# Kernel optimization log

Hardware: AMD Instinct MI355X
Metric: run time of the kernel (lower is better)

## Reference

```python
import jax, jax.numpy as jnp
import numpy as np

V = 1024      # token vocab
C = 8         # n_codebooks
T = 256       # seg_len
BP = 4        # block_pairs (n_latent_blocks)
K = 512       # latent_vocab_size (codebook entries)
E = 128       # emb_dim
D = 128       # latent_dim / d_model
BETA = 0.05
NB = 6 * BP   # decoder sequence length = 24
NH = 4
HD = D // NH
FF = 512
R = 8
IN_FLAT = NB * D
OUT = T * C * V
B = 32


def setup_inputs() -> dict:
    key = jax.random.key(0)
    ks = jax.random.split(key, 20)
    n = lambda i, shape, s=0.02: jax.random.normal(ks[i], shape, jnp.float32) * s
    return {
        "tokens_prev": jax.random.randint(ks[0], (B, T, C), 0, V, jnp.int32),
        "tokens_curr": jax.random.randint(ks[1], (B, T, C), 0, V, jnp.int32),
        "tokens_next": jax.random.randint(ks[2], (B, T, C), 0, V, jnp.int32),
        "emb": n(3, (V, E)),
        "conv1_w": n(4, (4 * D, E * C, 3)),
        "conv1_b": jnp.zeros((4 * D,), jnp.float32),
        "conv2_w": n(5, (2 * D, 4 * D, 1)),
        "conv2_b": jnp.zeros((2 * D,), jnp.float32),
        "cb_instru": jax.random.uniform(ks[6], (K, D), jnp.float32, -1.0 / K, 1.0 / K),
        "cb_vocal": jax.random.uniform(ks[7], (K, D), jnp.float32, -1.0 / K, 1.0 / K),
        "pos": n(8, (1, NB, D), 1.0),
        "attn_in_w": n(9, (3 * D, D)),
        "attn_in_b": jnp.zeros((3 * D,), jnp.float32),
        "attn_out_w": n(10, (D, D)),
        "attn_out_b": jnp.zeros((D,), jnp.float32),
        "ln1_g": jnp.ones((D,), jnp.float32),
        "ln1_b": jnp.zeros((D,), jnp.float32),
        "lin1_w": n(11, (FF, D)),
        "lin1_b": jnp.zeros((FF,), jnp.float32),
        "lin2_w": n(12, (D, FF)),
        "lin2_b": jnp.zeros((D,), jnp.float32),
        "ln2_g": jnp.ones((D,), jnp.float32),
        "ln2_b": jnp.zeros((D,), jnp.float32),
        "lora_a": n(13, (R, IN_FLAT), 0.01),
        "lora_b": n(14, (OUT, R), 0.01),
    }


def _conv1d(x, w, b, pad):
    # x: (B, Cin, L), w: (Cout, Cin, Kw)
    y = jax.lax.conv_general_dilated(x, w, window_strides=(1,), padding=[(pad, pad)],
                                     dimension_numbers=("NCH", "OIH", "NCH"))
    return y + b[None, :, None]


def _encode(tokens, emb, w1, b1, w2, b2):
    Bb, Tt, Cc = tokens.shape
    x = emb[tokens].reshape(Bb, Tt, -1).transpose(0, 2, 1)       # (B, C*E, T)
    x = jax.nn.relu(_conv1d(x, w1, b1, 1))                        # (B, 4D, T)
    x = jax.nn.relu(_conv1d(x, w2, b2, 0))                        # (B, 2D, T)
    # AdaptiveAvgPool1d(BP) with T % BP == 0 -> mean over contiguous chunks
    x = x.reshape(Bb, 2 * D, BP, Tt // BP).mean(-1).transpose(0, 2, 1)  # (B, BP, 2D)
    return x[..., :D], x[..., D:]


def _vq(z, codebook):
    # z: (B, N, D); eval-mode VQ (no EMA update)
    Bb, N, Dd = z.shape
    flat = z.reshape(-1, Dd)
    dist = (jnp.sum(flat * flat, axis=1, keepdims=True)
            - 2.0 * flat @ codebook.T
            + jnp.sum(codebook * codebook, axis=1))
    codes = jnp.argmin(dist, axis=1)
    z_q = codebook[codes].reshape(Bb, N, Dd)
    commit = jnp.mean((z - jax.lax.stop_gradient(z_q)) ** 2)
    loss = BETA * commit
    z_q_st = z + jax.lax.stop_gradient(z_q - z)
    return z_q_st, codes.reshape(Bb, N), loss


def _layer_norm(x, g, b):
    mu = x.mean(-1, keepdims=True)
    var = ((x - mu) ** 2).mean(-1, keepdims=True)
    return (x - mu) * jax.lax.rsqrt(var + 1e-5) * g + b


def _tf_layer(x, in_w, in_b, out_w, out_b, g1, b1, w1, bb1, w2, bb2, g2, b2):
    # Post-norm TransformerEncoderLayer (relu, eval/no-dropout). x: (B, S, D)
    Bb, S, Dd = x.shape
    qkv = x @ in_w.T + in_b
    q, k, v = jnp.split(qkv, 3, axis=-1)
    q = q.reshape(Bb, S, NH, HD).transpose(0, 2, 1, 3)
    k = k.reshape(Bb, S, NH, HD).transpose(0, 2, 1, 3)
    v = v.reshape(Bb, S, NH, HD).transpose(0, 2, 1, 3)
    attn = jax.nn.softmax(jnp.einsum("bhsd,bhtd->bhst", q, k) / np.sqrt(HD), axis=-1)
    o = jnp.einsum("bhst,bhtd->bhsd", attn, v).transpose(0, 2, 1, 3).reshape(Bb, S, Dd)
    x = _layer_norm(x + o @ out_w.T + out_b, g1, b1)
    ff = jax.nn.relu(x @ w1.T + bb1) @ w2.T + bb2
    return _layer_norm(x + ff, g2, b2)


def reference(tokens_prev, tokens_curr, tokens_next, emb, conv1_w, conv1_b,
              conv2_w, conv2_b, cb_instru, cb_vocal, pos, attn_in_w, attn_in_b,
              attn_out_w, attn_out_b, ln1_g, ln1_b, lin1_w, lin1_b, lin2_w,
              lin2_b, ln2_g, ln2_b, lora_a, lora_b):
    p_i, p_v = _encode(tokens_prev, emb, conv1_w, conv1_b, conv2_w, conv2_b)
    c_i, c_v = _encode(tokens_curr, emb, conv1_w, conv1_b, conv2_w, conv2_b)
    n_i, n_v = _encode(tokens_next, emb, conv1_w, conv1_b, conv2_w, conv2_b)
    p_i_q, _, l1 = _vq(p_i, cb_instru)
    c_i_q, _, l2 = _vq(c_i, cb_instru)
    n_i_q, _, l3 = _vq(n_i, cb_instru)
    p_v_q, _, l4 = _vq(p_v, cb_vocal)
    c_v_q, _, l5 = _vq(c_v, cb_vocal)
    n_v_q, _, l6 = _vq(n_v, cb_vocal)
    vq_loss = l1 + l2 + l3 + l4 + l5 + l6
    z = jnp.concatenate([p_i_q, p_v_q, c_i_q, c_v_q, n_i_q, n_v_q], axis=1)  # (B, 24, D)
    z = z + pos[:, :z.shape[1], :]
    z = _tf_layer(z, attn_in_w, attn_in_b, attn_out_w, attn_out_b,
                  ln1_g, ln1_b, lin1_w, lin1_b, lin2_w, lin2_b, ln2_g, ln2_b)
    Bb = z.shape[0]
    flat = z.reshape(Bb, -1)
    logits = (flat @ lora_a.T) @ lora_b.T          # (B, T*C*V)
    logits = logits.reshape(Bb, T, C, V)
    logp = jax.nn.log_softmax(logits, axis=-1)
    nll = -jnp.take_along_axis(logp, tokens_curr[..., None].astype(jnp.int32), axis=-1)
    recon_loss = nll.mean()
    total_loss = recon_loss + vq_loss
    return total_loss
```

## Files before the change

### kernel.cpp

```cpp
#include <hip/hip_runtime.h>
#include <hip/hip_bf16.h>
#include <cstdint>
#include <cstddef>

typedef __attribute__((ext_vector_type(8))) short short8;
typedef __attribute__((ext_vector_type(4))) float floatx4;


__device__ __forceinline__ ushort f2bf(float f) {
    union { float f; unsigned int u; } x; x.f = f;
    unsigned int r = (x.u + 0x7fffu + ((x.u >> 16) & 1u)) >> 16;
    return (ushort)r;
}
__device__ __forceinline__ float bf2f(ushort u) {
    union { unsigned int u; float f; } x; x.u = ((unsigned int)u) << 16;
    return x.f;
}

__global__ __launch_bounds__(256) void prep_all(
    const float* __restrict__ emb, const float* __restrict__ w1,
    const float* __restrict__ w2, const float* __restrict__ cbi,
    const float* __restrict__ cbv, const float* __restrict__ aiw,
    const float* __restrict__ aow, const float* __restrict__ l1w,
    const float* __restrict__ l2w,
    ushort* __restrict__ ebf, ushort* __restrict__ w1bf, ushort* __restrict__ w2bf,
    float* __restrict__ cbiT, float* __restrict__ cbvT,
    ushort* __restrict__ aiwbf, ushort* __restrict__ aowbf,
    ushort* __restrict__ l1wbf, ushort* __restrict__ l2wbf,
    float* __restrict__ accum)
{
    int idx = blockIdx.x * 256 + threadIdx.x;
    if (idx < 4) accum[idx] = 0.f;
    if (idx < 131072) {
        ebf[idx] = f2bf(emb[idx]);
    } else if (idx < 262144) {
        int j = idx - 131072; w2bf[j] = f2bf(w2[j]);
    } else if (idx < 327680) {
        int j = idx - 262144; cbiT[(j & 127) * 512 + (j >> 7)] = cbi[j];
    } else if (idx < 393216) {
        int j = idx - 327680; cbvT[(j & 127) * 512 + (j >> 7)] = cbv[j];
    } else if (idx < 442368) {
        int j = idx - 393216; aiwbf[j] = f2bf(aiw[j]);
    } else if (idx < 475136) {
        int j = idx - 442368; aowbf[j] = f2bf(aow[j]);
    } else if (idx < 540672) {
        int j = idx - 475136; l1wbf[j] = f2bf(l1w[j]);
    } else if (idx < 606208) {
        int j = idx - 540672; l2wbf[j] = f2bf(l2w[j]);
    } else if (idx < 2179072) {
        int j = idx - 606208;
        int e  = j & 127;
        int co = (j >> 7) & 511;
        int cc = (j >> 16) & 7;
        int kw = j >> 19;
        w1bf[j] = f2bf(w1[(co * 1024 + cc * 128 + e) * 3 + kw]);
    }
}

__global__ __launch_bounds__(512, 4) void conv1_mfma(
    const int* __restrict__ tp, const int* __restrict__ tcu, const int* __restrict__ tn,
    const ushort* __restrict__ ebf, const ushort* __restrict__ w1bf,
    const float* __restrict__ b1, ushort* __restrict__ y1)
{
    constexpr int LDA = 136;
    __shared__ ushort As[130 * LDA];
    __shared__ ushort Bs[128 * LDA];
    __shared__ int tokL[130 * 8];
    const int tid = threadIdx.x;
    const int bx = blockIdx.x;
    const int nb = bx & 3, mb = bx >> 2;
    const int set = mb >> 6, rem = mb & 63, bb = rem >> 1, t0 = (rem & 1) << 7;
    const int n0 = nb << 7;
    const int* tok = (set == 0) ? tp : ((set == 1) ? tcu : tn);

    for (int idx = tid; idx < 1040; idx += 512) {
        const int row = idx >> 3, cc = idx & 7;
        const int gt = t0 + row - 1;
        tokL[idx] = (gt >= 0 && gt < 256) ? tok[bb * 2048 + gt * 8 + cc] : -1;
    }

    const int w = tid >> 6, lane = tid & 63;
    const int wm = w & 1, wn = w >> 1;
    const int rA = lane & 15, q4 = lane >> 4;
    const int ch = tid & 15, rowst = tid >> 4;

    floatx4 acc[4][2];
    for (int mi = 0; mi < 4; ++mi)
        for (int ni = 0; ni < 2; ++ni)
            acc[mi][ni] = (floatx4)(0.0f);

    __syncthreads();

    for (int cc = 0; cc < 8; ++cc) {
        for (int p = 0; p < 5; ++p) {
            const int row = p * 32 + rowst;
            if (row < 130) {
                const int tk = tokL[row * 8 + cc];
                uint4 val = make_uint4(0u, 0u, 0u, 0u);
                if (tk >= 0) val = *(const uint4*)(ebf + tk * 128 + ch * 8);
                *(uint4*)(As + row * LDA + ch * 8) = val;
            }
        }
        for (int kw = 0; kw < 3; ++kw) {
            const ushort* wsrc = w1bf + ((size_t)((kw * 8 + cc) * 512 + n0)) * 128;
            for (int p = 0; p < 4; ++p) {
                const int row = p * 32 + rowst;
                *(uint4*)(Bs + row * LDA + ch * 8) = *(const uint4*)(wsrc + row * 128 + ch * 8);
            }
            __syncthreads();
            for (int ks = 0; ks < 4; ++ks) {
                const int k0 = ks * 32 + q4 * 8;
                short8 a[4], bfr[2];
                for (int mi = 0; mi < 4; ++mi)
                    a[mi] = *(const short8*)(As + (wm * 64 + mi * 16 + rA + kw) * LDA + k0);
                for (int ni = 0; ni < 2; ++ni)
                    bfr[ni] = *(const short8*)(Bs + (wn * 32 + ni * 16 + rA) * LDA + k0);
                for (int mi = 0; mi < 4; ++mi)
                    for (int ni = 0; ni < 2; ++ni)
                        acc[mi][ni] = __builtin_amdgcn_mfma_f32_16x16x32_bf16(
                            a[mi], bfr[ni], acc[mi][ni], 0, 0, 0);
            }
            __syncthreads();
        }
    }
    for (int ni = 0; ni < 2; ++ni) {
        const int co = n0 + wn * 32 + ni * 16 + rA;
        const float bias = b1[co];
        for (int mi = 0; mi < 4; ++mi) {
            for (int r = 0; r < 4; ++r) {
                const int t = t0 + wm * 64 + mi * 16 + q4 * 4 + r;
                float v = acc[mi][ni][r] + bias;
                v = v > 0.f ? v : 0.f;
                y1[((size_t)(set * 32 + bb) * 256 + t) * 512 + co] = f2bf(v);
            }
        }
    }
}

__global__ __launch_bounds__(512, 4) void conv2_mfma(
    const ushort* __restrict__ y1, const ushort* __restrict__ w2bf,
    const float* __restrict__ b2, float* __restrict__ y2)
{
    constexpr int LDA = 136;
    __shared__ ushort As[128 * LDA];
    __shared__ ushort Bs[128 * LDA];
    __shared__ float pool[256];
    const int tid = threadIdx.x;
    const int bx = blockIdx.x;
    const int nb = bx & 1, mb = bx >> 1;
    const int set = mb >> 6, rem = mb & 63, bb = rem >> 1, t0 = (rem & 1) << 7;
    const int n0 = nb << 7;
    const int w = tid >> 6, lane = tid & 63;
    const int wm = w & 1, wn = w >> 1;
    const int rA = lane & 15, q4 = lane >> 4;
    const int ch = tid & 15, rowst = tid >> 4;

    floatx4 acc[4][2];
    for (int mi = 0; mi < 4; ++mi)
        for (int ni = 0; ni < 2; ++ni)
            acc[mi][ni] = (floatx4)(0.0f);

    const size_t arowbase = ((size_t)(set * 32 + bb) * 256 + t0) * 512;
    for (int kc = 0; kc < 4; ++kc) {
        for (int p = 0; p < 4; ++p) {
            const int row = p * 32 + rowst;
            *(uint4*)(As + row * LDA + ch * 8) =
                *(const uint4*)(y1 + arowbase + (size_t)row * 512 + kc * 128 + ch * 8);
            *(uint4*)(Bs + row * LDA + ch * 8) =
                *(const uint4*)(w2bf + (size_t)(n0 + row) * 512 + kc * 128 + ch * 8);
        }
        __syncthreads();
        for (int ks = 0; ks < 4; ++ks) {
            const int k0 = ks * 32 + q4 * 8;
            short8 a[4], bfr[2];
            for (int mi = 0; mi < 4; ++mi)
                a[mi] = *(const short8*)(As + (wm * 64 + mi * 16 + rA) * LDA + k0);
            for (int ni = 0; ni < 2; ++ni)
                bfr[ni] = *(const short8*)(Bs + (wn * 32 + ni * 16 + rA) * LDA + k0);
            for (int mi = 0; mi < 4; ++mi)
                for (int ni = 0; ni < 2; ++ni)
                    acc[mi][ni] = __builtin_amdgcn_mfma_f32_16x16x32_bf16(
                        a[mi], bfr[ni], acc[mi][ni], 0, 0, 0);
        }
        __syncthreads();
    }
    for (int ni = 0; ni < 2; ++ni) {
        const int col = wn * 32 + ni * 16 + rA;
        const float bias = b2[n0 + col];
        float s = 0.f;
        for (int mi = 0; mi < 4; ++mi)
            for (int r = 0; r < 4; ++r) {
                float v = acc[mi][ni][r] + bias;
                s += v > 0.f ? v : 0.f;
            }
        s += __shfl_xor(s, 16);
        s += __shfl_xor(s, 32);
        if (q4 == 0) pool[wm * 128 + col] = s;
    }
    __syncthreads();
    if (tid < 256) {
        const int wrow = tid >> 7, col = tid & 127;
        const int p = (t0 >> 6) + wrow;
        y2[((size_t)(set * 32 + bb) * 4 + p) * 256 + n0 + col] = pool[tid] * (1.f / 64.f);
    }
}

__global__ __launch_bounds__(256) void vq_kernel(
    const float* __restrict__ y2, const float* __restrict__ cbiT, const float* __restrict__ cbvT,
    const float* __restrict__ cbi, const float* __restrict__ cbv,
    const float* __restrict__ pos, float* __restrict__ ztr, float* __restrict__ accum)
{
    const int q = blockIdx.x;
    const int tid = threadIdx.x;
    const int set = q >> 7, bb = (q >> 2) & 31, p = q & 3;
    __shared__ float zloc[256];
    __shared__ float bestv[4];
    __shared__ int   besti[4];
    __shared__ int   code_sh[2];
    __shared__ float wsum2[4];
    zloc[tid] = y2[(size_t)q * 256 + tid];
    __syncthreads();
    const int w = tid >> 6, lane = tid & 63;
    const int half = w >> 1, sub = w & 1;
    const float4* cbT4 = (const float4*)(half ? cbvT : cbiT);
    const float* zh = zloc + half * 128;
    const int k4 = sub * 64 + lane;
    float a0 = 0.f, a1 = 0.f, a2 = 0.f, a3 = 0.f;
    for (int d = 0; d < 128; ++d) {
        float4 v = cbT4[d * 128 + k4];
        const float z = zh[d];
        float d0 = z - v.x, d1 = z - v.y, d2 = z - v.z, d3 = z - v.w;
        a0 += d0 * d0; a1 += d1 * d1; a2 += d2 * d2; a3 += d3 * d3;
    }
    float best = a0; int bidx = k4 * 4;
    if (a1 < best) { best = a1; bidx = k4 * 4 + 1; }
    if (a2 < best) { best = a2; bidx = k4 * 4 + 2; }
    if (a3 < best) { best = a3; bidx = k4 * 4 + 3; }
    for (int off = 32; off > 0; off >>= 1) {
        float ov = __shfl_xor(best, off);
        int   oi = __shfl_xor(bidx, off);
        if (ov < best || (ov == best && oi < bidx)) { best = ov; bidx = oi; }
    }
    if (lane == 0) { bestv[w] = best; besti[w] = bidx; }
    __syncthreads();
    if (tid < 2) {
        float v0 = bestv[tid * 2], v1 = bestv[tid * 2 + 1];
        int   i0 = besti[tid * 2], i1 = besti[tid * 2 + 1];
        code_sh[tid] = (v1 < v0 || (v1 == v0 && i1 < i0)) ? i1 : i0;
    }
    __syncthreads();
    const int hh = tid >> 7, d = tid & 127;
    const int code = code_sh[hh];
    const float* cb = hh ? cbv : cbi;
    const float zq = cb[code * 128 + d];
    const float diff = zloc[hh * 128 + d] - zq;
    float sq = diff * diff;
    for (int off = 32; off > 0; off >>= 1) sq += __shfl_xor(sq, off);
    if (lane == 0) wsum2[w] = sq;
    const int s = (set * 2 + hh) * 4 + p;
    ztr[((size_t)bb * 24 + s) * 128 + d] = zq + pos[s * 128 + d];
    __syncthreads();
    if (tid == 0) atomicAdd(&accum[0], wsum2[0] + wsum2[1] + wsum2[2] + wsum2[3]);
}

__global__ __launch_bounds__(256) void tail_kernel(
    const float* __restrict__ ztr,
    const ushort* __restrict__ aiwbf, const float* __restrict__ aib,
    const ushort* __restrict__ aowbf, const float* __restrict__ aob,
    const float* __restrict__ g1, const float* __restrict__ be1,
    const ushort* __restrict__ l1wbf, const float* __restrict__ l1b,
    const ushort* __restrict__ l2wbf, const float* __restrict__ l2b,
    const float* __restrict__ g2, const float* __restrict__ be2,
    const float* __restrict__ lora_a, float* __restrict__ hbuf)
{
    __shared__ __align__(16) char LDSC[162304];
    float*  Xf  = (float*)LDSC;
    ushort* Abf = (ushort*)(LDSC + 12288);
    char*   S   = LDSC + 20992;
    ushort* Wq  = (ushort*)S;
    float*  QKV = (float*)(S + 104448);
    float*  Ssc = (float*)S;
    ushort* Wo  = (ushort*)S;
    ushort* W1  = (ushort*)S;
    ushort* Hbf = (ushort*)S;
    ushort* Wh  = (ushort*)(S + 34304);
    float*  ps  = (float*)(S + 104448);
    float*  pq  = (float*)(S + 104960);
    float*  muv = (float*)(S + 105472);
    float*  inv = (float*)(S + 105600);

    const int b = blockIdx.x;
    const int tid = threadIdx.x;
    const int w = tid >> 6, lane = tid & 63;
    const int rA = lane & 15, q4 = lane >> 4;

    for (int i = tid; i < 544; i += 256) ((uint4*)Abf)[i] = make_uint4(0u, 0u, 0u, 0u);
    __syncthreads();
    for (int i = tid; i < 3072; i += 256) {
        float v = ztr[(size_t)b * 3072 + i];
        Xf[i] = v;
        Abf[(i >> 7) * 136 + (i & 127)] = f2bf(v);
    }
    for (int i = tid; i < 6144; i += 256) {
        const int row = i >> 4, ch = i & 15;
        *(uint4*)(Wq + row * 136 + ch * 8) = *(const uint4*)(aiwbf + row * 128 + ch * 8);
    }
    __syncthreads();

    {
        floatx4 acc[2][6];
        for (int mi = 0; mi < 2; ++mi) for (int ni = 0; ni < 6; ++ni) acc[mi][ni] = (floatx4)(0.f);
        for (int ks = 0; ks < 4; ++ks) {
            const int k0 = ks * 32 + q4 * 8;
            short8 a[2];
            for (int mi = 0; mi < 2; ++mi)
                a[mi] = *(const short8*)(Abf + (mi * 16 + rA) * 136 + k0);
            for (int ni = 0; ni < 6; ++ni) {
                short8 bfr = *(const short8*)(Wq + ((w * 6 + ni) * 16 + rA) * 136 + k0);
                for (int mi = 0; mi < 2; ++mi)
                    acc[mi][ni] = __builtin_amdgcn_mfma_f32_16x16x32_bf16(a[mi], bfr, acc[mi][ni], 0, 0, 0);
            }
        }
        for (int ni = 0; ni < 6; ++ni) {
            const int col = (w * 6 + ni) * 16 + rA;
            const float bs = aib[col];
            for (int mi = 0; mi < 2; ++mi)
                for (int r = 0; r < 4; ++r) {
                    const int row = mi * 16 + q4 * 4 + r;
                    if (row < 24) QKV[row * 384 + col] = acc[mi][ni][r] + bs;
                }
        }
    }
    __syncthreads();

    {
        const int h = w;
        for (int l = 0; l < 9; ++l) {
            const int e = l * 64 + lane;
            const int i = e / 24, j = e - i * 24;
            float s = 0.f;
            for (int d = 0; d < 32; ++d)
                s += QKV[i * 384 + h * 32 + d] * QKV[j * 384 + 128 + h * 32 + d];
            Ssc[w * 576 + i * 24 + j] = s * 0.17677669529663687f;
        }
        __syncthreads();
        if (lane < 24) {
            float* row = Ssc + w * 576 + lane * 24;
            float m = row[0];
            for (int j = 1; j < 24; ++j) m = row[j] > m ? row[j] : m;
            float ssum = 0.f;
            for (int j = 0; j < 24; ++j) { float e = __expf(row[j] - m); row[j] = e; ssum += e; }
            float iv = 1.f / ssum;
            for (int j = 0; j < 24; ++j) row[j] *= iv;
        }
        __syncthreads();
        for (int l = 0; l < 12; ++l) {
            const int idx = l * 64 + lane;
            const int s = idx >> 5, d = idx & 31;
            float a = 0.f;
            for (int j = 0; j < 24; ++j)
                a += Ssc[w * 576 + s * 24 + j] * QKV[j * 384 + 256 + h * 32 + d];
            Abf[s * 136 + h * 32 + d] = f2bf(a);
        }
    }
    __syncthreads();

    for (int i = tid; i < 2048; i += 256) {
        const int row = i >> 4, ch = i & 15;
        *(uint4*)(Wo + row * 136 + ch * 8) = *(const uint4*)(aowbf + row * 128 + ch * 8);
    }
    __syncthreads();
    {
        floatx4 acc[2][2];
        for (int mi = 0; mi < 2; ++mi) for (int ni = 0; ni < 2; ++ni) acc[mi][ni] = (floatx4)(0.f);
        for (int ks = 0; ks < 4; ++ks) {
            const int k0 = ks * 32 + q4 * 8;
            short8 a[2];
            for (int mi = 0; mi < 2; ++mi)
                a[mi] = *(const short8*)(Abf + (mi * 16 + rA) * 136 + k0);
            for (int ni = 0; ni < 2; ++ni) {
                short8 bfr = *(const short8*)(Wo + ((w * 2 + ni) * 16 + rA) * 136 + k0);
                for (int mi = 0; mi < 2; ++mi)
                    acc[mi][ni] = __builtin_amdgcn_mfma_f32_16x16x32_bf16(a[mi], bfr, acc[mi][ni], 0, 0, 0);
            }
        }
        for (int ni = 0; ni < 2; ++ni) {
            const int col = (w * 2 + ni) * 16 + rA;
            const float bs = aob[col];
            for (int mi = 0; mi < 2; ++mi)
                for (int r = 0; r < 4; ++r) {
                    const int row = mi * 16 + q4 * 4 + r;
                    acc[mi][ni][r] += bs + (row < 24 ? Xf[row * 128 + col] : 0.f);
                }
        }
        for (int mi = 0; mi < 2; ++mi)
            for (int r = 0; r < 4; ++r) {
                float s  = acc[mi][0][r] + acc[mi][1][r];
                float sq = acc[mi][0][r] * acc[mi][0][r] + acc[mi][1][r] * acc[mi][1][r];
                for (int off = 1; off < 16; off <<= 1) { s += __shfl_xor(s, off); sq += __shfl_xor(sq, off); }
                if (rA == 0) { const int rl = mi * 16 + q4 * 4 + r; ps[rl * 4 + w] = s; pq[rl * 4 + w] = sq; }
            }
        __syncthreads();
        if (tid < 32) {
            float s  = ps[tid * 4] + ps[tid * 4 + 1] + ps[tid * 4 + 2] + ps[tid * 4 + 3];
            float sq = pq[tid * 4] + pq[tid * 4 + 1] + pq[tid * 4 + 2] + pq[tid * 4 + 3];
            float mu = s * (1.f / 128.f);
            float var = sq * (1.f / 128.f) - mu * mu;
            muv[tid] = mu; inv[tid] = rsqrtf(var + 1e-5f);
        }
        __syncthreads();
        for (int ni = 0; ni < 2; ++ni) {
            const int col = (w * 2 + ni) * 16 + rA;
            const float gg = g1[col], bb2 = be1[col];
            for (int mi = 0; mi < 2; ++mi)
                for (int r = 0; r < 4; ++r) {
                    const int rl = mi * 16 + q4 * 4 + r;
                    if (rl < 24) {
                        float v = (acc[mi][ni][r] - muv[rl]) * inv[rl] * gg + bb2;
                        Xf[rl * 128 + col] = v;
                        Abf[rl * 136 + col] = f2bf(v);
                    }
                }
        }
    }
    __syncthreads();

    for (int i = tid; i < 8192; i += 256) {
        const int row = i >> 4, ch = i & 15;
        *(uint4*)(W1 + row * 136 + ch * 8) = *(const uint4*)(l1wbf + row * 128 + ch * 8);
    }
    __syncthreads();
    {
        floatx4 acc[2][8];
        for (int mi = 0; mi < 2; ++mi) for (int ni = 0; ni < 8; ++ni) acc[mi][ni] = (floatx4)(0.f);
        for (int ks = 0; ks < 4; ++ks) {
            const int k0 = ks * 32 + q4 * 8;
            short8 a[2];
            for (int mi = 0; mi < 2; ++mi)
                a[mi] = *(const short8*)(Abf + (mi * 16 + rA) * 136 + k0);
            for (int ni = 0; ni < 8; ++ni) {
                short8 bfr = *(const short8*)(W1 + ((w * 8 + ni) * 16 + rA) * 136 + k0);
                for (int mi = 0; mi < 2; ++mi)
                    acc[mi][ni] = __builtin_amdgcn_mfma_f32_16x16x32_bf16(a[mi], bfr, acc[mi][ni], 0, 0, 0);
            }
        }
        __syncthreads();
        for (int i = tid; i < 536; i += 256) ((uint4*)(Hbf + 24 * 536))[i] = make_uint4(0u, 0u, 0u, 0u);
        for (int ni = 0; ni < 8; ++ni) {
            const int col = (w * 8 + ni) * 16 + rA;
            const float bs = l1b[col];
            for (int mi = 0; mi < 2; ++mi)
                for (int r = 0; r < 4; ++r) {
                    const int row = mi * 16 + q4 * 4 + r;
                    if (row < 24) {
                        float v = acc[mi][ni][r] + bs;
                        Hbf[row * 536 + col] = f2bf(v > 0.f ? v : 0.f);
                    }
                }
        }
    }
    __syncthreads();

    {
        floatx4 acc[2][2];
        for (int mi = 0; mi < 2; ++mi) for (int ni = 0; ni < 2; ++ni) acc[mi][ni] = (floatx4)(0.f);
        for (int kh = 0; kh < 2; ++kh) {
            for (int i = tid; i < 4096; i += 256) {
                const int row = i >> 5, ch = i & 31;
                *(uint4*)(Wh + row * 264 + ch * 8) =
                    *(const uint4*)(l2wbf + row * 512 + kh * 256 + ch * 8);
            }
            __syncthreads();
            for (int ks = 0; ks < 8; ++ks) {
                const int k0 = ks * 32 + q4 * 8;
                short8 a[2];
                for (int mi = 0; mi < 2; ++mi)
                    a[mi] = *(const short8*)(Hbf + (mi * 16 + rA) * 536 + kh * 256 + k0);
                for (int ni = 0; ni < 2; ++ni) {
                    short8 bfr = *(const short8*)(Wh + ((w * 2 + ni) * 16 + rA) * 264 + k0);
                    for (int mi = 0; mi < 2; ++mi)
                        acc[mi][ni] = __builtin_amdgcn_mfma_f32_16x16x32_bf16(a[mi], bfr, acc[mi][ni], 0, 0, 0);
                }
            }
            __syncthreads();
        }
        for (int ni = 0; ni < 2; ++ni) {
            const int col = (w * 2 + ni) * 16 + rA;
            const float bs = l2b[col];
            for (int mi = 0; mi < 2; ++mi)
                for (int r = 0; r < 4; ++r) {
                    const int row = mi * 16 + q4 * 4 + r;
                    acc[mi][ni][r] += bs + (row < 24 ? Xf[row * 128 + col] : 0.f);
                }
        }
        for (int mi = 0; mi < 2; ++mi)
            for (int r = 0; r < 4; ++r) {
                float s  = acc[mi][0][r] + acc[mi][1][r];
                float sq = acc[mi][0][r] * acc[mi][0][r] + acc[mi][1][r] * acc[mi][1][r];
                for (int off = 1; off < 16; off <<= 1) { s += __shfl_xor(s, off); sq += __shfl_xor(sq, off); }
                if (rA == 0) { const int rl = mi * 16 + q4 * 4 + r; ps[rl * 4 + w] = s; pq[rl * 4 + w] = sq; }
            }
        __syncthreads();
        if (tid < 32) {
            float s  = ps[tid * 4] + ps[tid * 4 + 1] + ps[tid * 4 + 2] + ps[tid * 4 + 3];
            float sq = pq[tid * 4] + pq[tid * 4 + 1] + pq[tid * 4 + 2] + pq[tid * 4 + 3];
            float mu = s * (1.f / 128.f);
            float var = sq * (1.f / 128.f) - mu * mu;
            muv[tid] = mu; inv[tid] = rsqrtf(var + 1e-5f);
        }
        __syncthreads();
        for (int ni = 0; ni < 2; ++ni) {
            const int col = (w * 2 + ni) * 16 + rA;
            const float gg = g2[col], bb2 = be2[col];
            for (int mi = 0; mi < 2; ++mi)
                for (int r = 0; r < 4; ++r) {
                    const int rl = mi * 16 + q4 * 4 + r;
                    if (rl < 24)
                        Xf[rl * 128 + col] = (acc[mi][ni][r] - muv[rl]) * inv[rl] * gg + bb2;
                }
        }
    }
    __syncthreads();

    for (int rr = 0; rr < 2; ++rr) {
        const int r = w + rr * 4;
        float a = 0.f;
        for (int i = lane; i < 3072; i += 64)
            a += lora_a[(size_t)r * 3072 + i] * Xf[i];
        for (int off = 32; off > 0; off >>= 1) a += __shfl_xor(a, off);
        if (lane == 0) hbuf[b * 8 + r] = a;
    }
}

__global__ __launch_bounds__(256) void logits_kernel(
    const float* __restrict__ hbuf, const float* __restrict__ lora_b,
    const int* __restrict__ tokc, float* __restrict__ accum, float* __restrict__ out)
{
    const int tid = threadIdx.x;
    const int tcb = blockIdx.x;
    __shared__ float hl[256];
    __shared__ float wsum[4];
    __shared__ float ltok;
    hl[tid] = hbuf[tid];
    float wr[4][8];
    for (int i = 0; i < 4; ++i) {
        const float4* pw = (const float4*)(lora_b + ((size_t)tcb * 1024 + tid + 256 * i) * 8);
        float4 x = pw[0], y = pw[1];
        wr[i][0] = x.x; wr[i][1] = x.y; wr[i][2] = x.z; wr[i][3] = x.w;
        wr[i][4] = y.x; wr[i][5] = y.y; wr[i][6] = y.z; wr[i][7] = y.w;
    }
    __syncthreads();
    float nll = 0.f;
    for (int bb = 0; bb < 32; ++bb) {
        const int tv = tokc[bb * 2048 + tcb];
        const float* h = hl + bb * 8;
        float h0 = h[0], h1 = h[1], h2 = h[2], h3 = h[3];
        float h4 = h[4], h5 = h[5], h6 = h[6], h7 = h[7];
        float sl = 0.f;
        for (int i = 0; i < 4; ++i) {
            float lg = h0 * wr[i][0] + h1 * wr[i][1] + h2 * wr[i][2] + h3 * wr[i][3]
                     + h4 * wr[i][4] + h5 * wr[i][5] + h6 * wr[i][6] + h7 * wr[i][7];
            sl += __expf(lg);
            if (tid + 256 * i == tv) ltok = lg;
        }
        for (int off = 32; off > 0; off >>= 1) sl += __shfl_xor(sl, off);
        if ((tid & 63) == 0) wsum[tid >> 6] = sl;
        __syncthreads();
        if (tid == 0) nll += logf(wsum[0] + wsum[1] + wsum[2] + wsum[3]) - ltok;
        __syncthreads();
    }
    if (tid == 0) {
        atomicAdd(&accum[1], nll);
        __threadfence();
        unsigned int prev = atomicAdd((unsigned int*)(accum + 2), 1u);
        if (prev == 2047u) {
            float vq  = atomicAdd(&accum[0], 0.f);
            float rec = atomicAdd(&accum[1], 0.f);
            out[0] = rec * (1.f / 65536.f) + 0.05f * vq * (1.f / 16384.f);
        }
    }
}

extern "C" void kernel_launch(void* const* d_in, const int* in_sizes, int n_in,
                              void* d_out, int out_size, void* d_ws, size_t ws_size,
                              hipStream_t stream) {
    const int*   tp   = (const int*)d_in[0];
    const int*   tcu  = (const int*)d_in[1];
    const int*   tn   = (const int*)d_in[2];
    const float* emb  = (const float*)d_in[3];
    const float* w1   = (const float*)d_in[4];
    const float* b1   = (const float*)d_in[5];
    const float* w2   = (const float*)d_in[6];
    const float* b2   = (const float*)d_in[7];
    const float* cbi  = (const float*)d_in[8];
    const float* cbv  = (const float*)d_in[9];
    const float* pos  = (const float*)d_in[10];
    const float* aiw  = (const float*)d_in[11];
    const float* aib  = (const float*)d_in[12];
    const float* aow  = (const float*)d_in[13];
    const float* aob  = (const float*)d_in[14];
    const float* g1   = (const float*)d_in[15];
    const float* be1  = (const float*)d_in[16];
    const float* l1w  = (const float*)d_in[17];
    const float* l1b  = (const float*)d_in[18];
    const float* l2w  = (const float*)d_in[19];
    const float* l2b  = (const float*)d_in[20];
    const float* g2   = (const float*)d_in[21];
    const float* be2  = (const float*)d_in[22];
    const float* lra  = (const float*)d_in[23];
    const float* lrb  = (const float*)d_in[24];

    char* wsb = (char*)d_ws;
    ushort* ebf  = (ushort*)(wsb + 0);
    ushort* w1bf = (ushort*)(wsb + 262144);
    ushort* w2bf = (ushort*)(wsb + 3407872);
    float*  cbiT = (float*)(wsb + 3670016);
    float*  cbvT = (float*)(wsb + 3932160);
    ushort* y1   = (ushort*)(wsb + 4194304);
    float*  y2   = (float*)(wsb + 29360128);
    float*  ztr  = (float*)(wsb + 29753344);
    float*  hbuf = (float*)(wsb + 30146560);
    float*  accum= (float*)(wsb + 30147584);
    ushort* aiwbf= (ushort*)(wsb + 30147648);
    ushort* aowbf= (ushort*)(wsb + 30245952);
    ushort* l1wbf= (ushort*)(wsb + 30278720);
    ushort* l2wbf= (ushort*)(wsb + 30409792);
    if (ws_size < 30540864) return;

    prep_all<<<8512, 256, 0, stream>>>(emb, w1, w2, cbi, cbv, aiw, aow, l1w, l2w,
                                       ebf, w1bf, w2bf, cbiT, cbvT,
                                       aiwbf, aowbf, l1wbf, l2wbf, accum);
    conv1_mfma<<<768, 512, 0, stream>>>(tp, tcu, tn, ebf, w1bf, b1, y1);
    conv2_mfma<<<384, 512, 0, stream>>>(y1, w2bf, b2, y2);
    vq_kernel<<<384, 256, 0, stream>>>(y2, cbiT, cbvT, cbi, cbv, pos, ztr, accum);
    tail_kernel<<<32, 256, 0, stream>>>(ztr, aiwbf, aib, aowbf, aob, g1, be1,
                                        l1wbf, l1b, l2wbf, l2b, g2, be2, lra, hbuf);
    logits_kernel<<<2048, 256, 0, stream>>>(hbuf, lrb, tcu, accum, (float*)d_out);
}
```

Before: 409.8 us.

## Replace conv1 GEMM with precomputed embedding-weight table and token gather

```diff
diff --git a/kernel.cpp b/kernel.cpp
--- a/kernel.cpp
+++ b/kernel.cpp
@@ -57,6 +57,108 @@
     }
 }
 
+__global__ __launch_bounds__(512) void ubuild_kernel(
+    const ushort* __restrict__ ebf, const ushort* __restrict__ w1bf,
+    ushort* __restrict__ U)
+{
+    constexpr int LDA = 136;
+    __shared__ ushort As[128 * LDA];
+    __shared__ ushort Bs[128 * LDA];
+    const int tid = threadIdx.x;
+    const int bx = blockIdx.x;
+    const int kc = bx >> 5, rem = bx & 31, mt = rem >> 2, nt = rem & 3;
+    const int v0 = mt << 7, co0 = nt << 7;
+    const int w = tid >> 6, lane = tid & 63;
+    const int wm = w & 1, wn = w >> 1;
+    const int rA = lane & 15, q4 = lane >> 4;
+    const int ch = tid & 15, rowst = tid >> 4;
+
+    for (int p = 0; p < 4; ++p) {
+        const int row = p * 32 + rowst;
+        *(uint4*)(As + row * LDA + ch * 8) =
+            *(const uint4*)(ebf + (size_t)(v0 + row) * 128 + ch * 8);
+        *(uint4*)(Bs + row * LDA + ch * 8) =
+            *(const uint4*)(w1bf + (size_t)kc * 65536 + (size_t)(co0 + row) * 128 + ch * 8);
+    }
+    __syncthreads();
+
+    floatx4 acc[4][2];
+    for (int mi = 0; mi < 4; ++mi)
+        for (int ni = 0; ni < 2; ++ni)
+            acc[mi][ni] = (floatx4)(0.0f);
+    for (int ks = 0; ks < 4; ++ks) {
+        const int k0 = ks * 32 + q4 * 8;
+        short8 a[4], bfr[2];
+        for (int mi = 0; mi < 4; ++mi)
+            a[mi] = *(const short8*)(As + (wm * 64 + mi * 16 + rA) * LDA + k0);
+        for (int ni = 0; ni < 2; ++ni)
+            bfr[ni] = *(const short8*)(Bs + (wn * 32 + ni * 16 + rA) * LDA + k0);
+        for (int mi = 0; mi < 4; ++mi)
+            for (int ni = 0; ni < 2; ++ni)
+                acc[mi][ni] = __builtin_amdgcn_mfma_f32_16x16x32_bf16(
+                    a[mi], bfr[ni], acc[mi][ni], 0, 0, 0);
+    }
+    for (int ni = 0; ni < 2; ++ni) {
+        const int col = co0 + wn * 32 + ni * 16 + rA;
+        for (int mi = 0; mi < 4; ++mi)
+            for (int r = 0; r < 4; ++r) {
+                const int row = v0 + wm * 64 + mi * 16 + q4 * 4 + r;
+                U[((size_t)kc * 1024 + row) * 512 + col] = f2bf(acc[mi][ni][r]);
+            }
+    }
+}
+
+__global__ __launch_bounds__(256) void conv1_gather(
+    const int* __restrict__ tp, const int* __restrict__ tcu, const int* __restrict__ tn,
+    const ushort* __restrict__ U, const float* __restrict__ b1,
+    ushort* __restrict__ y1)
+{
+    __shared__ int tokL[34 * 8];
+    const int bx = blockIdx.x;
+    const int set = bx >> 8, bb = (bx >> 3) & 31, pp = bx & 7;
+    const int t0 = pp << 5;
+    const int* tok = (set == 0) ? tp : ((set == 1) ? tcu : tn);
+    const int tid = threadIdx.x;
+    const int w = tid >> 6, lane = tid & 63;
+
+    for (int idx = tid; idx < 272; idx += 256) {
+        const int row = idx >> 3, cc = idx & 7;
+        const int gt = t0 + row - 1;
+        tokL[idx] = (gt >= 0 && gt < 256) ? tok[bb * 2048 + gt * 8 + cc] : -1;
+    }
+    float bias[8];
+    {
+        const float4* b4 = (const float4*)(b1 + lane * 8);
+        float4 x = b4[0], y = b4[1];
+        bias[0] = x.x; bias[1] = x.y; bias[2] = x.z; bias[3] = x.w;
+        bias[4] = y.x; bias[5] = y.y; bias[6] = y.z; bias[7] = y.w;
+    }
+    __syncthreads();
+
+    const size_t outbase = ((size_t)(set * 32 + bb) * 256 + t0) * 512 + lane * 8;
+    for (int tl = 0; tl < 8; ++tl) {
+        const int row = w * 8 + tl;
+        float acc[8];
+        for (int j = 0; j < 8; ++j) acc[j] = bias[j];
+        for (int kw = 0; kw < 3; ++kw) {
+            const int* trow = tokL + (row + kw) * 8;
+            for (int cc = 0; cc < 8; ++cc) {
+                const int u = trow[cc];
+                if (u >= 0) {
+                    const short8 s = *(const short8*)(U + (((size_t)(kw * 8 + cc) * 1024 + u) * 512 + lane * 8));
+                    for (int j = 0; j < 8; ++j) acc[j] += bf2f((ushort)s[j]);
+                }
+            }
+        }
+        ushort o[8];
+        for (int j = 0; j < 8; ++j) {
+            float v = acc[j];
+            o[j] = f2bf(v > 0.f ? v : 0.f);
+        }
+        *(uint4*)(y1 + outbase + (size_t)row * 512) = *(const uint4*)o;
+    }
+}
+
 __global__ __launch_bounds__(512, 4) void conv1_mfma(
     const int* __restrict__ tp, const int* __restrict__ tcu, const int* __restrict__ tn,
     const ushort* __restrict__ ebf, const ushort* __restrict__ w1bf,
@@ -625,12 +727,19 @@
     ushort* aowbf= (ushort*)(wsb + 30245952);
     ushort* l1wbf= (ushort*)(wsb + 30278720);
     ushort* l2wbf= (ushort*)(wsb + 30409792);
+    ushort* U    = (ushort*)(wsb + 30541824);
     if (ws_size < 30540864) return;
+    const bool use_u = (ws_size >= 55707648);
 
     prep_all<<<8512, 256, 0, stream>>>(emb, w1, w2, cbi, cbv, aiw, aow, l1w, l2w,
                                        ebf, w1bf, w2bf, cbiT, cbvT,
                                        aiwbf, aowbf, l1wbf, l2wbf, accum);
-    conv1_mfma<<<768, 512, 0, stream>>>(tp, tcu, tn, ebf, w1bf, b1, y1);
+    if (use_u) {
+        ubuild_kernel<<<768, 512, 0, stream>>>(ebf, w1bf, U);
+        conv1_gather<<<768, 256, 0, stream>>>(tp, tcu, tn, U, b1, y1);
+    } else {
+        conv1_mfma<<<768, 512, 0, stream>>>(tp, tcu, tn, ebf, w1bf, b1, y1);
+    }
     conv2_mfma<<<384, 512, 0, stream>>>(y1, w2bf, b2, y2);
     vq_kernel<<<384, 256, 0, stream>>>(y2, cbiT, cbvT, cbi, cbv, pos, ztr, accum);
     tail_kernel<<<32, 256, 0, stream>>>(ztr, aiwbf, aib, aowbf, aob, g1, be1,
```

New measurement: 416.9 us. No clear change (+1.8%).

## Widen tail kernel to 1024 threads and coalesce conv1 weight prep reads

Applied to the files above, without the earlier changes.

```diff
diff --git a/kernel.cpp b/kernel.cpp
--- a/kernel.cpp
+++ b/kernel.cpp
@@ -30,7 +30,7 @@
     float* __restrict__ accum)
 {
     int idx = blockIdx.x * 256 + threadIdx.x;
-    if (idx < 4) accum[idx] = 0.f;
+    if (idx < 16) accum[idx] = 0.f;
     if (idx < 131072) {
         ebf[idx] = f2bf(emb[idx]);
     } else if (idx < 262144) {
@@ -47,13 +47,16 @@
         int j = idx - 475136; l1wbf[j] = f2bf(l1w[j]);
     } else if (idx < 606208) {
         int j = idx - 540672; l2wbf[j] = f2bf(l2w[j]);
-    } else if (idx < 2179072) {
+    } else if (idx < 1130496) {
         int j = idx - 606208;
         int e  = j & 127;
-        int co = (j >> 7) & 511;
-        int cc = (j >> 16) & 7;
-        int kw = j >> 19;
-        w1bf[j] = f2bf(w1[(co * 1024 + cc * 128 + e) * 3 + kw]);
+        int cc = (j >> 7) & 7;
+        int co = j >> 10;
+        const float* src = w1 + ((size_t)co * 1024 + cc * 128 + e) * 3;
+        float v0 = src[0], v1 = src[1], v2 = src[2];
+        w1bf[((size_t)(0 * 8 + cc) * 512 + co) * 128 + e] = f2bf(v0);
+        w1bf[((size_t)(1 * 8 + cc) * 512 + co) * 128 + e] = f2bf(v1);
+        w1bf[((size_t)(2 * 8 + cc) * 512 + co) * 128 + e] = f2bf(v2);
     }
 }
 
@@ -263,7 +266,7 @@
     if (tid == 0) atomicAdd(&accum[0], wsum2[0] + wsum2[1] + wsum2[2] + wsum2[3]);
 }
 
-__global__ __launch_bounds__(256) void tail_kernel(
+__global__ __launch_bounds__(1024) void tail_kernel(
     const float* __restrict__ ztr,
     const ushort* __restrict__ aiwbf, const float* __restrict__ aib,
     const ushort* __restrict__ aowbf, const float* __restrict__ aob,
@@ -281,254 +284,246 @@
     float*  QKV = (float*)(S + 104448);
     float*  Ssc = (float*)S;
     ushort* Wo  = (ushort*)S;
+    float*  psA = (float*)(S + 36864);
+    float*  pqA = (float*)(S + 37888);
+    float*  muvA= (float*)(S + 38912);
+    float*  invA= (float*)(S + 39040);
     ushort* W1  = (ushort*)S;
     ushort* Hbf = (ushort*)S;
-    ushort* Wh  = (ushort*)(S + 34304);
-    float*  ps  = (float*)(S + 104448);
-    float*  pq  = (float*)(S + 104960);
-    float*  muv = (float*)(S + 105472);
-    float*  inv = (float*)(S + 105600);
+    ushort* Wh  = (ushort*)(S + 33280);
+    float*  psB = (float*)(S + 100864);
+    float*  pqB = (float*)(S + 101888);
+    float*  muvB= (float*)(S + 102912);
+    float*  invB= (float*)(S + 103040);
+    float*  psL = (float*)(S + 103168);
 
     const int b = blockIdx.x;
     const int tid = threadIdx.x;
     const int w = tid >> 6, lane = tid & 63;
     const int rA = lane & 15, q4 = lane >> 4;
-
-    for (int i = tid; i < 544; i += 256) ((uint4*)Abf)[i] = make_uint4(0u, 0u, 0u, 0u);
-    __syncthreads();
-    for (int i = tid; i < 3072; i += 256) {
+    const int ch = tid & 15;
+
+    if (tid < 544) ((uint4*)Abf)[tid] = make_uint4(0u, 0u, 0u, 0u);
+    __syncthreads();
+    for (int i = tid; i < 3072; i += 1024) {
         float v = ztr[(size_t)b * 3072 + i];
         Xf[i] = v;
         Abf[(i >> 7) * 136 + (i & 127)] = f2bf(v);
     }
-    for (int i = tid; i < 6144; i += 256) {
-        const int row = i >> 4, ch = i & 15;
-        *(uint4*)(Wq + row * 136 + ch * 8) = *(const uint4*)(aiwbf + row * 128 + ch * 8);
+    for (int i = tid; i < 6144; i += 1024) {
+        const int row = i >> 4, c = i & 15;
+        *(uint4*)(Wq + row * 136 + c * 8) = *(const uint4*)(aiwbf + row * 128 + c * 8);
     }
     __syncthreads();
 
     {
-        floatx4 acc[2][6];
-        for (int mi = 0; mi < 2; ++mi) for (int ni = 0; ni < 6; ++ni) acc[mi][ni] = (floatx4)(0.f);
+        floatx4 acc[3];
+        int mI[3], nI[3];
+        for (int i = 0; i < 3; ++i) {
+            const int t = w + 16 * i;
+            mI[i] = t / 24; nI[i] = t % 24;
+            acc[i] = (floatx4)(0.f);
+        }
         for (int ks = 0; ks < 4; ++ks) {
             const int k0 = ks * 32 + q4 * 8;
-            short8 a[2];
-            for (int mi = 0; mi < 2; ++mi)
-                a[mi] = *(const short8*)(Abf + (mi * 16 + rA) * 136 + k0);
-            for (int ni = 0; ni < 6; ++ni) {
-                short8 bfr = *(const short8*)(Wq + ((w * 6 + ni) * 16 + rA) * 136 + k0);
-                for (int mi = 0; mi < 2; ++mi)
-                    acc[mi][ni] = __builtin_amdgcn_mfma_f32_16x16x32_bf16(a[mi], bfr, acc[mi][ni], 0, 0, 0);
-            }
-        }
-        for (int ni = 0; ni < 6; ++ni) {
-            const int col = (w * 6 + ni) * 16 + rA;
+            for (int i = 0; i < 3; ++i) {
+                short8 a = *(const short8*)(Abf + (mI[i] * 16 + rA) * 136 + k0);
+                short8 bf = *(const short8*)(Wq + (nI[i] * 16 + rA) * 136 + k0);
+                acc[i] = __builtin_amdgcn_mfma_f32_16x16x32_bf16(a, bf, acc[i], 0, 0, 0);
+            }
+        }
+        for (int i = 0; i < 3; ++i) {
+            const int col = nI[i] * 16 + rA;
             const float bs = aib[col];
-            for (int mi = 0; mi < 2; ++mi)
-                for (int r = 0; r < 4; ++r) {
-                    const int row = mi * 16 + q4 * 4 + r;
-                    if (row < 24) QKV[row * 384 + col] = acc[mi][ni][r] + bs;
-                }
-        }
-    }
-    __syncthreads();
-
-    {
-        const int h = w;
-        for (int l = 0; l < 9; ++l) {
-            const int e = l * 64 + lane;
-            const int i = e / 24, j = e - i * 24;
+            for (int r = 0; r < 4; ++r) {
+                const int row = mI[i] * 16 + q4 * 4 + r;
+                if (row < 24) QKV[row * 384 + col] = acc[i][r] + bs;
+            }
+        }
+    }
+    __syncthreads();
+
+    for (int it = 0; it < 3; ++it) {
+        const int e = it * 1024 + tid;
+        if (e < 2304) {
+            const int h = e / 576, rem = e % 576, i = rem / 24, j = rem % 24;
             float s = 0.f;
             for (int d = 0; d < 32; ++d)
                 s += QKV[i * 384 + h * 32 + d] * QKV[j * 384 + 128 + h * 32 + d];
-            Ssc[w * 576 + i * 24 + j] = s * 0.17677669529663687f;
-        }
-        __syncthreads();
-        if (lane < 24) {
-            float* row = Ssc + w * 576 + lane * 24;
-            float m = row[0];
-            for (int j = 1; j < 24; ++j) m = row[j] > m ? row[j] : m;
-            float ssum = 0.f;
-            for (int j = 0; j < 24; ++j) { float e = __expf(row[j] - m); row[j] = e; ssum += e; }
-            float iv = 1.f / ssum;
-            for (int j = 0; j < 24; ++j) row[j] *= iv;
-        }
-        __syncthreads();
-        for (int l = 0; l < 12; ++l) {
-            const int idx = l * 64 + lane;
-            const int s = idx >> 5, d = idx & 31;
+            Ssc[h * 576 + i * 24 + j] = s * 0.17677669529663687f;
+        }
+    }
+    __syncthreads();
+    if (tid < 96) {
+        const int h = tid / 24, r = tid % 24;
+        float* row = Ssc + h * 576 + r * 24;
+        float m = row[0];
+        for (int j = 1; j < 24; ++j) m = row[j] > m ? row[j] : m;
+        float ssum = 0.f;
+        for (int j = 0; j < 24; ++j) { float e = __expf(row[j] - m); row[j] = e; ssum += e; }
+        float iv = 1.f / ssum;
+        for (int j = 0; j < 24; ++j) row[j] *= iv;
+    }
+    __syncthreads();
+    for (int it = 0; it < 3; ++it) {
+        const int idx = it * 1024 + tid;
+        const int s = idx >> 7, dcol = idx & 127, h = dcol >> 5, d = dcol & 31;
+        if (s < 24) {
             float a = 0.f;
             for (int j = 0; j < 24; ++j)
-                a += Ssc[w * 576 + s * 24 + j] * QKV[j * 384 + 256 + h * 32 + d];
-            Abf[s * 136 + h * 32 + d] = f2bf(a);
-        }
-    }
-    __syncthreads();
-
-    for (int i = tid; i < 2048; i += 256) {
-        const int row = i >> 4, ch = i & 15;
-        *(uint4*)(Wo + row * 136 + ch * 8) = *(const uint4*)(aowbf + row * 128 + ch * 8);
-    }
-    __syncthreads();
+                a += Ssc[h * 576 + s * 24 + j] * QKV[j * 384 + 256 + h * 32 + d];
+            Abf[s * 136 + dcol] = f2bf(a);
+        }
+    }
+    __syncthreads();
+
+    for (int i = tid; i < 2048; i += 1024) {
+        const int row = i >> 4, c = i & 15;
+        *(uint4*)(Wo + row * 136 + c * 8) = *(const uint4*)(aowbf + row * 128 + c * 8);
+    }
+    __syncthreads();
+
     {
-        floatx4 acc[2][2];
-        for (int mi = 0; mi < 2; ++mi) for (int ni = 0; ni < 2; ++ni) acc[mi][ni] = (floatx4)(0.f);
+        const int m = w & 1, n = w >> 1;
+        floatx4 acc = (floatx4)(0.f);
         for (int ks = 0; ks < 4; ++ks) {
             const int k0 = ks * 32 + q4 * 8;
-            short8 a[2];
-            for (int mi = 0; mi < 2; ++mi)
-                a[mi] = *(const short8*)(Abf + (mi * 16 + rA) * 136 + k0);
-            for (int ni = 0; ni < 2; ++ni) {
-                short8 bfr = *(const short8*)(Wo + ((w * 2 + ni) * 16 + rA) * 136 + k0);
-                for (int mi = 0; mi < 2; ++mi)
-                    acc[mi][ni] = __builtin_amdgcn_mfma_f32_16x16x32_bf16(a[mi], bfr, acc[mi][ni], 0, 0, 0);
-            }
-        }
-        for (int ni = 0; ni < 2; ++ni) {
-            const int col = (w * 2 + ni) * 16 + rA;
-            const float bs = aob[col];
-            for (int mi = 0; mi < 2; ++mi)
-                for (int r = 0; r < 4; ++r) {
-                    const int row = mi * 16 + q4 * 4 + r;
-                    acc[mi][ni][r] += bs + (row < 24 ? Xf[row * 128 + col] : 0.f);
-                }
-        }
-        for (int mi = 0; mi < 2; ++mi)
-            for (int r = 0; r < 4; ++r) {
-                float s  = acc[mi][0][r] + acc[mi][1][r];
-                float sq = acc[mi][0][r] * acc[mi][0][r] + acc[mi][1][r] * acc[mi][1][r];
-                for (int off = 1; off < 16; off <<= 1) { s += __shfl_xor(s, off); sq += __shfl_xor(sq, off); }
-                if (rA == 0) { const int rl = mi * 16 + q4 * 4 + r; ps[rl * 4 + w] = s; pq[rl * 4 + w] = sq; }
-            }
+            short8 a = *(const short8*)(Abf + (m * 16 + rA) * 136 + k0);
+            short8 bf = *(const short8*)(Wo + (n * 16 + rA) * 136 + k0);
+            acc = __builtin_amdgcn_mfma_f32_16x16x32_bf16(a, bf, acc, 0, 0, 0);
+        }
+        const int col = n * 16 + rA;
+        const float bs = aob[col];
+        for (int r = 0; r < 4; ++r) {
+            const int row = m * 16 + q4 * 4 + r;
+            acc[r] += bs + (row < 24 ? Xf[row * 128 + col] : 0.f);
+        }
+        float s4 = 0.f, q4s = 0.f;
+        for (int r = 0; r < 4; ++r) {
+            float s = acc[r], sq = acc[r] * acc[r];
+            for (int off = 1; off < 16; off <<= 1) { s += __shfl_xor(s, off); sq += __shfl_xor(sq, off); }
+            if (rA == 0) {
+                const int rl = m * 16 + q4 * 4 + r;
+                psA[rl * 8 + n] = s; pqA[rl * 8 + n] = sq;
+            }
+        }
+        (void)s4; (void)q4s;
         __syncthreads();
         if (tid < 32) {
-            float s  = ps[tid * 4] + ps[tid * 4 + 1] + ps[tid * 4 + 2] + ps[tid * 4 + 3];
-            float sq = pq[tid * 4] + pq[tid * 4 + 1] + pq[tid * 4 + 2] + pq[tid * 4 + 3];
+            float s = 0.f, sq = 0.f;
+            for (int j = 0; j < 8; ++j) { s += psA[tid * 8 + j]; sq += pqA[tid * 8 + j]; }
             float mu = s * (1.f / 128.f);
             float var = sq * (1.f / 128.f) - mu * mu;
-            muv[tid] = mu; inv[tid] = rsqrtf(var + 1e-5f);
-        }
-        __syncthreads();
-        for (int ni = 0; ni < 2; ++ni) {
-            const int col = (w * 2 + ni) * 16 + rA;
-            const float gg = g1[col], bb2 = be1[col];
-            for (int mi = 0; mi < 2; ++mi)
-                for (int r = 0; r < 4; ++r) {
-                    const int rl = mi * 16 + q4 * 4 + r;
-                    if (rl < 24) {
-                        float v = (acc[mi][ni][r] - muv[rl]) * inv[rl] * gg + bb2;
-                        Xf[rl * 128 + col] = v;
-                        Abf[rl * 136 + col] = f2bf(v);
-                    }
-                }
-        }
-    }
-    __syncthreads();
-
-    for (int i = tid; i < 8192; i += 256) {
-        const int row = i >> 4, ch = i & 15;
-        *(uint4*)(W1 + row * 136 + ch * 8) = *(const uint4*)(l1wbf + row * 128 + ch * 8);
-    }
-    __syncthreads();
+            muvA[tid] = mu; invA[tid] = rsqrtf(var + 1e-5f);
+        }
+        __syncthreads();
+        const float gg = g1[col], bb2 = be1[col];
+        for (int r = 0; r < 4; ++r) {
+            const int rl = m * 16 + q4 * 4 + r;
+            if (rl < 24) {
+                float v = (acc[r] - muvA[rl]) * invA[rl] * gg + bb2;
+                Xf[rl * 128 + col] = v;
+                Abf[rl * 136 + col] = f2bf(v);
+            }
+        }
+    }
+    __syncthreads();
+
+    for (int i = tid; i < 8192; i += 1024) {
+        const int row = i >> 4, c = i & 15;
+        *(uint4*)(W1 + row * 136 + c * 8) = *(const uint4*)(l1wbf + row * 128 + c * 8);
+    }
+    __syncthreads();
+
     {
-        floatx4 acc[2][8];
-        for (int mi = 0; mi < 2; ++mi) for (int ni = 0; ni < 8; ++ni) acc[mi][ni] = (floatx4)(0.f);
+        const int m = w & 1, n0b = w >> 1;
+        floatx4 acc[4];
+        for (int i = 0; i < 4; ++i) acc[i] = (floatx4)(0.f);
         for (int ks = 0; ks < 4; ++ks) {
             const int k0 = ks * 32 + q4 * 8;
-            short8 a[2];
-            for (int mi = 0; mi < 2; ++mi)
-                a[mi] = *(const short8*)(Abf + (mi * 16 + rA) * 136 + k0);
-            for (int ni = 0; ni < 8; ++ni) {
-                short8 bfr = *(const short8*)(W1 + ((w * 8 + ni) * 16 + rA) * 136 + k0);
-                for (int mi = 0; mi < 2; ++mi)
-                    acc[mi][ni] = __builtin_amdgcn_mfma_f32_16x16x32_bf16(a[mi], bfr, acc[mi][ni], 0, 0, 0);
-            }
-        }
-        __syncthreads();
-        for (int i = tid; i < 536; i += 256) ((uint4*)(Hbf + 24 * 536))[i] = make_uint4(0u, 0u, 0u, 0u);
-        for (int ni = 0; ni < 8; ++ni) {
-            const int col = (w * 8 + ni) * 16 + rA;
+            short8 a = *(const short8*)(Abf + (m * 16 + rA) * 136 + k0);
+            for (int i = 0; i < 4; ++i) {
+                const int n = n0b + i * 8;
+                short8 bf = *(const short8*)(W1 + (n * 16 + rA) * 136 + k0);
+                acc[i] = __builtin_amdgcn_mfma_f32_16x16x32_bf16(a, bf, acc[i], 0, 0, 0);
+            }
+        }
+        __syncthreads();
+        for (int i = 0; i < 4; ++i) {
+            const int col = (n0b + i * 8) * 16 + rA;
             const float bs = l1b[col];
-            for (int mi = 0; mi < 2; ++mi)
-                for (int r = 0; r < 4; ++r) {
-                    const int row = mi * 16 + q4 * 4 + r;
-                    if (row < 24) {
-                        float v = acc[mi][ni][r] + bs;
-                        Hbf[row * 536 + col] = f2bf(v > 0.f ? v : 0.f);
-                    }
+            for (int r = 0; r < 4; ++r) {
+                const int row = m * 16 + q4 * 4 + r;
+                if (row < 24) {
+                    float v = acc[i][r] + bs;
+                    Hbf[row * 520 + col] = f2bf(v > 0.f ? v : 0.f);
                 }
+            }
         }
     }
     __syncthreads();
 
     {
-        floatx4 acc[2][2];
-        for (int mi = 0; mi < 2; ++mi) for (int ni = 0; ni < 2; ++ni) acc[mi][ni] = (floatx4)(0.f);
+        const int m = w & 1, n = w >> 1;
+        floatx4 acc = (floatx4)(0.f);
         for (int kh = 0; kh < 2; ++kh) {
-            for (int i = tid; i < 4096; i += 256) {
-                const int row = i >> 5, ch = i & 31;
-                *(uint4*)(Wh + row * 264 + ch * 8) =
-                    *(const uint4*)(l2wbf + row * 512 + kh * 256 + ch * 8);
+            if (kh) __syncthreads();
+            for (int i = tid; i < 4096; i += 1024) {
+                const int row = i >> 5, c = i & 31;
+                *(uint4*)(Wh + row * 264 + c * 8) =
+                    *(const uint4*)(l2wbf + row * 512 + kh * 256 + c * 8);
             }
             __syncthreads();
             for (int ks = 0; ks < 8; ++ks) {
                 const int k0 = ks * 32 + q4 * 8;
-                short8 a[2];
-                for (int mi = 0; mi < 2; ++mi)
-                    a[mi] = *(const short8*)(Hbf + (mi * 16 + rA) * 536 + kh * 256 + k0);
-                for (int ni = 0; ni < 2; ++ni) {
-                    short8 bfr = *(const short8*)(Wh + ((w * 2 + ni) * 16 + rA) * 264 + k0);
-                    for (int mi = 0; mi < 2; ++mi)
-                        acc[mi][ni] = __builtin_amdgcn_mfma_f32_16x16x32_bf16(a[mi], bfr, acc[mi][ni], 0, 0, 0);
-                }
-            }
-            __syncthreads();
-        }
-        for (int ni = 0; ni < 2; ++ni) {
-            const int col = (w * 2 + ni) * 16 + rA;
-            const float bs = l2b[col];
-            for (int mi = 0; mi < 2; ++mi)
-                for (int r = 0; r < 4; ++r) {
-                    const int row = mi * 16 + q4 * 4 + r;
-                    acc[mi][ni][r] += bs + (row < 24 ? Xf[row * 128 + col] : 0.f);
-                }
-        }
-        for (int mi = 0; mi < 2; ++mi)
-            for (int r = 0; r < 4; ++r) {
-                float s  = acc[mi][0][r] + acc[mi][1][r];
-                float sq = acc[mi][0][r] * acc[mi][0][r] + acc[mi][1][r] * acc[mi][1][r];
-                for (int off = 1; off < 16; off <<= 1) { s += __shfl_xor(s, off); sq += __shfl_xor(sq, off); }
-                if (rA == 0) { const int rl = mi * 16 + q4 * 4 + r; ps[rl * 4 + w] = s; pq[rl * 4 + w] = sq; }
-            }
+                short8 a = *(const short8*)(Hbf + (m * 16 + rA) * 520 + kh * 256 + k0);
+                short8 bf = *(const short8*)(Wh + (n * 16 + rA) * 264 + k0);
+                acc = __builtin_amdgcn_mfma_f32_16x16x32_bf16(a, bf, acc, 0, 0, 0);
+            }
+        }
+        const int col = n * 16 + rA;
+        const float bs = l2b[col];
+        for (int r = 0; r < 4; ++r) {
+            const int row = m * 16 + q4 * 4 + r;
+            acc[r] += bs + (row < 24 ? Xf[row * 128 + col] : 0.f);
+        }
+        for (int r = 0; r < 4; ++r) {
+            float s = acc[r], sq = acc[r] * acc[r];
+            for (int off = 1; off < 16; off <<= 1) { s += __shfl_xor(s, off); sq += __shfl_xor(sq, off); }
+            if (rA == 0) {
+                const int rl = m * 16 + q4 * 4 + r;
+                psB[rl * 8 + n] = s; pqB[rl * 8 + n] = sq;
+            }
+        }
         __syncthreads();
         if (tid < 32) {
-            float s  = ps[tid * 4] + ps[tid * 4 + 1] + ps[tid * 4 + 2] + ps[tid * 4 + 3];
-            float sq = pq[tid * 4] + pq[tid * 4 + 1] + pq[tid * 4 + 2] + pq[tid * 4 + 3];
+            float s = 0.f, sq = 0.f;
+            for (int j = 0; j < 8; ++j) { s += psB[tid * 8 + j]; sq += pqB[tid * 8 + j]; }
             float mu = s * (1.f / 128.f);
             float var = sq * (1.f / 128.f) - mu * mu;
-            muv[tid] = mu; inv[tid] = rsqrtf(var + 1e-5f);
-        }
-        __syncthreads();
-        for (int ni = 0; ni < 2; ++ni) {
-            const int col = (w * 2 + ni) * 16 + rA;
-            const float gg = g2[col], bb2 = be2[col];
-            for (int mi = 0; mi < 2; ++mi)
-                for (int r = 0; r < 4; ++r) {
-                    const int rl = mi * 16 + q4 * 4 + r;
-                    if (rl < 24)
-                        Xf[rl * 128 + col] = (acc[mi][ni][r] - muv[rl]) * inv[rl] * gg + bb2;
-                }
-        }
-    }
-    __syncthreads();
-
-    for (int rr = 0; rr < 2; ++rr) {
-        const int r = w + rr * 4;
+            muvB[tid] = mu; invB[tid] = rsqrtf(var + 1e-5f);
+        }
+        __syncthreads();
+        const float gg = g2[col], bb2 = be2[col];
+        for (int r = 0; r < 4; ++r) {
+            const int rl = m * 16 + q4 * 4 + r;
+            if (rl < 24)
+                Xf[rl * 128 + col] = (acc[r] - muvB[rl]) * invB[rl] * gg + bb2;
+        }
+    }
+    __syncthreads();
+
+    {
+        const int r = w & 7, seg = w >> 3;
         float a = 0.f;
-        for (int i = lane; i < 3072; i += 64)
-            a += lora_a[(size_t)r * 3072 + i] * Xf[i];
+        for (int k = 0; k < 24; ++k) {
+            const int idx = seg * 1536 + k * 64 + lane;
+            a += lora_a[(size_t)r * 3072 + idx] * Xf[idx];
+        }
         for (int off = 32; off > 0; off >>= 1) a += __shfl_xor(a, off);
-        if (lane == 0) hbuf[b * 8 + r] = a;
+        if (lane == 0) psL[r * 2 + seg] = a;
+        __syncthreads();
+        if (tid < 8) hbuf[b * 8 + tid] = psL[tid * 2] + psL[tid * 2 + 1];
     }
 }
 
@@ -627,13 +622,13 @@
     ushort* l2wbf= (ushort*)(wsb + 30409792);
     if (ws_size < 30540864) return;
 
-    prep_all<<<8512, 256, 0, stream>>>(emb, w1, w2, cbi, cbv, aiw, aow, l1w, l2w,
+    prep_all<<<4416, 256, 0, stream>>>(emb, w1, w2, cbi, cbv, aiw, aow, l1w, l2w,
                                        ebf, w1bf, w2bf, cbiT, cbvT,
                                        aiwbf, aowbf, l1wbf, l2wbf, accum);
     conv1_mfma<<<768, 512, 0, stream>>>(tp, tcu, tn, ebf, w1bf, b1, y1);
     conv2_mfma<<<384, 512, 0, stream>>>(y1, w2bf, b2, y2);
     vq_kernel<<<384, 256, 0, stream>>>(y2, cbiT, cbvT, cbi, cbv, pos, ztr, accum);
-    tail_kernel<<<32, 256, 0, stream>>>(ztr, aiwbf, aib, aowbf, aob, g1, be1,
-                                        l1wbf, l1b, l2wbf, l2b, g2, be2, lra, hbuf);
+    tail_kernel<<<32, 1024, 0, stream>>>(ztr, aiwbf, aib, aowbf, aob, g1, be1,
+                                         l1wbf, l1b, l2wbf, l2b, g2, be2, lra, hbuf);
     logits_kernel<<<2048, 256, 0, stream>>>(hbuf, lrb, tcu, accum, (float*)d_out);
 }
```

Result: faster. 361.0 us (-11.9%).
